# Kernel optimization log

Measured on AMD Instinct MI355X. Metric: run time of the kernel, lower is better.

## Reference

```python
import jax, jax.numpy as jnp
import numpy as np
import itertools

# hyperparameters (match init_kwargs cfg)
V_SIZE = 32000; D = 768; H = 12; NL = 2
K_BITS = 4; L_TAB = 4; M_COPIES = 2; HID = 3072
DK = D // H; R = 1 << K_BITS; EPS = 1e-6; RMS_EPS = 1e-5

def _protos_T():
    # corners of the {-1,+1}^K hypercube, transposed -> [K, R]
    corners = np.array(list(itertools.product([-1.0, 1.0], repeat=K_BITS)), dtype=np.float32)
    return jnp.asarray(corners.T)

def setup_inputs() -> dict:
    key = jax.random.key(0)
    ks = jax.random.split(key, 14)
    s = 0.02
    return {
        "in_idx": jax.random.randint(ks[0], (1, 1024), 0, V_SIZE),
        "tok_emb": jax.random.normal(ks[1], (V_SIZE, D), jnp.float32) * s,
        "norm1_w": jnp.ones((NL, D), jnp.float32),
        "qw": jax.random.normal(ks[2], (NL, D, D), jnp.float32) * s,
        "kw": jax.random.normal(ks[3], (NL, D, D), jnp.float32) * s,
        "vw": jax.random.normal(ks[4], (NL, D, D), jnp.float32) * s,
        "ow": jax.random.normal(ks[5], (NL, D, D), jnp.float32) * s,
        "ob": jnp.zeros((NL, D), jnp.float32),
        "norm2_w": jnp.ones((NL, D), jnp.float32),
        "ff_w1": jax.random.normal(ks[6], (NL, D, HID), jnp.float32) * s,
        "ff_w2": jax.random.normal(ks[7], (NL, D, HID), jnp.float32) * s,
        "ff_w3": jax.random.normal(ks[8], (NL, HID, D), jnp.float32) * s,
        "final_norm_w": jnp.ones((D,), jnp.float32),
        "out_w": jax.random.normal(ks[9], (D, V_SIZE), jnp.float32) * s,
        "planes_T": jax.random.normal(ks[10], (NL, M_COPIES, DK, L_TAB * K_BITS), jnp.float32),
    }

def _rmsnorm(x, w):
    return x * jax.lax.rsqrt(jnp.mean(x * x, axis=-1, keepdims=True) + RMS_EPS) * w

def _race_attention(h, qw, kw, vw, ow, ob, planes, protos_T):
    B, T, _ = h.shape
    Q = (h @ qw).reshape(B, T, H, DK)
    Kt = (h @ kw).reshape(B, T, H, DK)
    Vt = (h @ vw).reshape(B, T, H, DK)
    # RoPE (split-even/odd, concat halves variant, start position 0)
    theta = 10000.0 ** (-jnp.arange(0, DK, 2, dtype=jnp.float32) / DK)
    freq = jnp.arange(T, dtype=jnp.float32)[:, None] * theta[None, :]  # [T, DK/2]
    sin = jnp.sin(freq)[None, :, None, :]
    cos = jnp.cos(freq)[None, :, None, :]
    def rope(z):
        e, o = z[..., ::2], z[..., 1::2]
        return jnp.concatenate([e * cos - o * sin, e * sin + o * cos], axis=-1)
    Q, Kt = rope(Q), rope(Kt)
    to_hb = lambda z: jnp.transpose(z, (0, 2, 1, 3)).reshape(B * H, T, DK)
    Qh, Kh, Vh = to_hb(Q), to_hb(Kt), to_hb(Vt)
    N = M_COPIES * B * H
    scale = jnp.sqrt(jnp.float32(DK))
    # random-plane projections per model copy m: [M, BH, T, L*K]
    projK = jnp.einsum('ntd,mds->mnts', Kh, planes).reshape(N, T, L_TAB, K_BITS)
    projQ = jnp.einsum('ntd,mds->mnts', Qh, planes).reshape(N, T, L_TAB, K_BITS)
    probsK = jax.nn.softmax((jnp.tanh(projK) / scale) @ protos_T, axis=-1)  # [N,T,L,R]
    probsQ = jax.nn.softmax((jnp.tanh(projQ) / scale) @ protos_T, axis=-1)
    Vn = jnp.broadcast_to(Vh[None], (M_COPIES, B * H, T, DK)).reshape(N, T, DK)
    # causal prefix sums over time
    A_pref = jnp.cumsum(probsK, axis=1)                                     # [N,T,L,R]
    B_pref = jnp.cumsum(probsK[..., None] * Vn[:, :, None, None, :], axis=1)  # [N,T,L,R,DK]
    E_pref = B_pref / (A_pref[..., None] + EPS)
    out2 = jnp.einsum('ntlr,ntlrd->ntd', probsQ, E_pref)                    # [N,T,DK]
    out_h = out2.reshape(M_COPIES, B, H, T, DK).transpose(0, 1, 3, 2, 4)    # [M,B,T,H,DK]
    m = out_h.mean(axis=0)                                                  # [B,T,H,DK]
    # faithful to the source: permute to [B,H,T,DK] then row-major reshape to [B,T,H*DK]
    out = jnp.transpose(m, (0, 2, 1, 3)).reshape(B, T, H * DK)
    return out @ ow + ob

def reference(in_idx, tok_emb, norm1_w, qw, kw, vw, ow, ob, norm2_w,
              ff_w1, ff_w2, ff_w3, final_norm_w, out_w, planes_T):
    protos_T = _protos_T()
    x = tok_emb[in_idx]  # [B,T,D]
    for l in range(NL):
        h = _rmsnorm(x, norm1_w[l])
        x = x + _race_attention(h, qw[l], kw[l], vw[l], ow[l], ob[l], planes_T[l], protos_T)
        h = _rmsnorm(x, norm2_w[l])
        x = x + (jax.nn.silu(h @ ff_w1[l]) * (h @ ff_w2[l])) @ ff_w3[l]
    x = _rmsnorm(x, final_norm_w)
    return x @ out_w  # logits [B,T,V]
```

## Files before the change

### kernel.cpp

```cpp
#include <hip/hip_runtime.h>
#include <hip/hip_bf16.h>

#define T_SEQ 1024
#define D_MODEL 768
#define QKVW 2304
#define NHEAD 12
#define NLAYER 2
#define MCOPY 2
#define HID_DIM 3072
#define VSIZE 32000
#define NCH 32
#define TL 32

typedef __attribute__((ext_vector_type(8))) short short8;
typedef __attribute__((ext_vector_type(4))) float f32x4;

__device__ __forceinline__ short f2bf(float f) {
  unsigned u = __builtin_bit_cast(unsigned, f);
  u = (u + 0x7FFFu + ((u >> 16) & 1u)) >> 16;
  return (short)u;
}

__global__ __launch_bounds__(64) void stc_k(float* __restrict__ stc) {
  int t = blockIdx.x;
  int i = threadIdx.x;
  if (i < 32) {
    float theta = powf(10000.0f, -(float)i / 32.0f);
    float s, c;
    sincosf((float)t * theta, &s, &c);
    stc[t * 64 + 2 * i] = c;
    stc[t * 64 + 2 * i + 1] = s;
  }
}

__global__ __launch_bounds__(256) void embed_norm_k(const int* __restrict__ idx,
                                                    const float* __restrict__ emb,
                                                    const float* __restrict__ w,
                                                    float* __restrict__ x,
                                                    short* __restrict__ out) {
  int t = blockIdx.x, tid = threadIdx.x;
  int r = idx[t];
  float v[3];
  float ss = 0.f;
  #pragma unroll
  for (int j = 0; j < 3; ++j) {
    int i = tid + j * 256;
    float val = emb[(size_t)r * D_MODEL + i];
    x[(size_t)t * D_MODEL + i] = val;
    v[j] = val;
    ss += val * val;
  }
  __shared__ float red[256];
  red[tid] = ss; __syncthreads();
  for (int s = 128; s > 0; s >>= 1) {
    if (tid < s) red[tid] += red[tid + s];
    __syncthreads();
  }
  float inv = rsqrtf(red[0] / (float)D_MODEL + 1e-5f);
  #pragma unroll
  for (int j = 0; j < 3; ++j) {
    int i = tid + j * 256;
    out[(size_t)t * D_MODEL + i] = f2bf(v[j] * inv * w[i]);
  }
}

__global__ __launch_bounds__(256) void add_norm_k(float* __restrict__ x,
                                                  const float* __restrict__ parts,
                                                  int nparts,
                                                  const float* __restrict__ bias,
                                                  const float* __restrict__ w,
                                                  short* __restrict__ out) {
  int t = blockIdx.x, tid = threadIdx.x;
  float v[3];
  float ss = 0.f;
  #pragma unroll
  for (int j = 0; j < 3; ++j) {
    int i = tid + j * 256;
    float val = x[(size_t)t * D_MODEL + i];
    if (bias) val += bias[i];
    for (int p = 0; p < nparts; ++p)
      val += parts[(size_t)p * (T_SEQ * D_MODEL) + (size_t)t * D_MODEL + i];
    v[j] = val;
    ss += val * val;
  }
  __shared__ float red[256];
  red[tid] = ss; __syncthreads();
  for (int s = 128; s > 0; s >>= 1) {
    if (tid < s) red[tid] += red[tid + s];
    __syncthreads();
  }
  float inv = rsqrtf(red[0] / (float)D_MODEL + 1e-5f);
  #pragma unroll
  for (int j = 0; j < 3; ++j) {
    int i = tid + j * 256;
    if (nparts || bias) x[(size_t)t * D_MODEL + i] = v[j];
    out[(size_t)t * D_MODEL + i] = f2bf(v[j] * inv * w[i]);
  }
}

__device__ __forceinline__ void tr_tile(const float* __restrict__ W,
                                        short* __restrict__ WT, int K, int N,
                                        int n0, int k0, int tx, int ty) {
  __shared__ float tile[32][33];
  #pragma unroll
  for (int i = 0; i < 4; ++i)
    tile[ty + 8 * i][tx] = W[(size_t)(k0 + ty + 8 * i) * N + n0 + tx];
  __syncthreads();
  #pragma unroll
  for (int i = 0; i < 4; ++i)
    WT[(size_t)(n0 + ty + 8 * i) * K + k0 + tx] = f2bf(tile[tx][ty + 8 * i]);
}

#define SQ_W  ((size_t)D_MODEL * D_MODEL)
#define FF_W  ((size_t)D_MODEL * HID_DIM)
#define LAYER_W (4 * SQ_W + 3 * FF_W)

__global__ __launch_bounds__(256) void transpose_sq8(const float* __restrict__ qw,
                                                     const float* __restrict__ kw,
                                                     const float* __restrict__ vw,
                                                     const float* __restrict__ ow,
                                                     short* __restrict__ WB) {
  int z = blockIdx.z, layer = z >> 2, which = z & 3;
  const float* W = (which == 0) ? qw : (which == 1) ? kw : (which == 2) ? vw : ow;
  W += (size_t)layer * SQ_W;
  short* WT = WB + (size_t)layer * LAYER_W + (size_t)which * SQ_W;
  tr_tile(W, WT, D_MODEL, D_MODEL, blockIdx.x * 32, blockIdx.y * 32,
          threadIdx.x, threadIdx.y);
}

__global__ __launch_bounds__(256) void transpose_ff12(const float* __restrict__ W1g,
                                                      const float* __restrict__ W2g,
                                                      short* __restrict__ WB) {
  __shared__ float tile[32][33];
  int layer = blockIdx.z;
  const float* W1 = W1g + (size_t)layer * FF_W;
  const float* W2 = W2g + (size_t)layer * FF_W;
  short* WT = WB + (size_t)layer * LAYER_W + 4 * SQ_W;
  int tx = threadIdx.x, ty = threadIdx.y;
  int n0 = blockIdx.x * 32, k0 = blockIdx.y * 32;
  int h0 = n0 >> 1;
  const float* src = (tx < 16) ? (W1 + h0 + tx) : (W2 + h0 + (tx - 16));
  #pragma unroll
  for (int i = 0; i < 4; ++i)
    tile[ty + 8 * i][tx] = src[(size_t)(k0 + ty + 8 * i) * HID_DIM];
  __syncthreads();
  #pragma unroll
  for (int i = 0; i < 4; ++i) {
    int n = ty + 8 * i;
    WT[(size_t)(n0 + n) * D_MODEL + k0 + tx] = f2bf(tile[tx][n]);
  }
}

__global__ __launch_bounds__(256) void transpose_f3(const float* __restrict__ W3g,
                                                    short* __restrict__ WB) {
  int layer = blockIdx.z;
  const float* W = W3g + (size_t)layer * FF_W;
  short* WT = WB + (size_t)layer * LAYER_W + 4 * SQ_W + 2 * FF_W;
  tr_tile(W, WT, HID_DIM, D_MODEL, blockIdx.x * 32, blockIdx.y * 32,
          threadIdx.x, threadIdx.y);
}

__global__ __launch_bounds__(256) void transpose_head(const float* __restrict__ W,
                                                      short* __restrict__ WT) {
  tr_tile(W, WT, D_MODEL, VSIZE, blockIdx.x * 32, blockIdx.y * 32,
          threadIdx.x, threadIdx.y);
}

template<int NROW32>
__device__ __forceinline__ void stage_rows(const short* __restrict__ gbase,
                                           int ldK, short* lds, int tid) {
  #pragma unroll
  for (int j = 0; j < NROW32; ++j) {
    int r = j * 32 + (tid >> 3);
    int s = tid & 7;
    const short* gp = gbase + (size_t)r * ldK + (((s ^ (r & 7))) << 3);
    short* lp = lds + j * 2048 + tid * 8;
    __builtin_amdgcn_global_load_lds((const __attribute__((address_space(1))) void*)gp,
                                     (__attribute__((address_space(3))) void*)lp,
                                     16, 0, 0);
  }
}

__device__ __forceinline__ short8 frag_ld(const short* lds, int row, int sl) {
  return *(const short8*)(lds + row * 64 + ((sl ^ (row & 7)) << 3));
}

template<int MODE>
__global__ __launch_bounds__(256) void gemm_t(const short* __restrict__ A,
                                              const short* __restrict__ Bt,
                                              float* __restrict__ Cf,
                                              short* __restrict__ Cs,
                                              int N, int K) {
  __shared__ short As[2][128 * 64];
  __shared__ short Bs[2][128 * 64];
  int tid = threadIdx.x;
  int lane = tid & 63;
  int wave = tid >> 6;
  int wr = wave >> 1, wc = wave & 1;
  int l15 = lane & 15, kg = lane >> 4;

  int cpx = gridDim.x >> 3;
  int wg = (blockIdx.x & 7) * cpx + (blockIdx.x >> 3);
  int row0 = (wg & 7) * 128;
  int col0 = (wg >> 3) * 128;

  int kn = K / gridDim.y;
  int koff = blockIdx.y * kn;
  const short* Ab = A + (size_t)row0 * K + koff;
  const short* Bb = Bt + (size_t)col0 * K + koff;
  int nt = kn >> 6;

  f32x4 acc[4][4] = {};

  stage_rows<4>(Ab, K, As[0], tid);
  stage_rows<4>(Bb, K, Bs[0], tid);
  __syncthreads();

  int cur = 0;
  for (int t = 0; t < nt; ++t) {
    if (t + 1 < nt) {
      stage_rows<4>(Ab + (t + 1) * 64, K, As[cur ^ 1], tid);
      stage_rows<4>(Bb + (t + 1) * 64, K, Bs[cur ^ 1], tid);
    }
    const short* Ac = As[cur];
    const short* Bc = Bs[cur];
    #pragma unroll
    for (int kk = 0; kk < 2; ++kk) {
      short8 af[4], bf4[4];
      #pragma unroll
      for (int m = 0; m < 4; ++m)
        af[m] = frag_ld(Ac, wr * 64 + m * 16 + l15, 4 * kk + kg);
      #pragma unroll
      for (int n = 0; n < 4; ++n)
        bf4[n] = frag_ld(Bc, wc * 64 + n * 16 + l15, 4 * kk + kg);
      #pragma unroll
      for (int m = 0; m < 4; ++m)
        #pragma unroll
        for (int n = 0; n < 4; ++n)
          acc[m][n] = __builtin_amdgcn_mfma_f32_16x16x32_bf16(af[m], bf4[n], acc[m][n], 0, 0, 0);
    }
    __syncthreads();
    cur ^= 1;
  }

  int rbase = (lane >> 4) * 4;
  if constexpr (MODE == 2) {
    int base = col0 + wc * 64;
    #pragma unroll
    for (int p = 0; p < 2; ++p) {
      int h = (base >> 1) + p * 16 + l15;
      #pragma unroll
      for (int m = 0; m < 4; ++m) {
        #pragma unroll
        for (int r = 0; r < 4; ++r) {
          int row = row0 + wr * 64 + m * 16 + rbase + r;
          float g1 = acc[m][2 * p][r];
          float g2 = acc[m][2 * p + 1][r];
          Cs[(size_t)row * HID_DIM + h] = f2bf((g1 / (1.f + expf(-g1))) * g2);
        }
      }
    }
  } else {
    float* Co = Cf;
    if constexpr (MODE == 1) Co += (size_t)blockIdx.y * T_SEQ * N;
    #pragma unroll
    for (int n = 0; n < 4; ++n) {
      int col = col0 + wc * 64 + n * 16 + l15;
      #pragma unroll
      for (int m = 0; m < 4; ++m) {
        #pragma unroll
        for (int r = 0; r < 4; ++r) {
          int row = row0 + wr * 64 + m * 16 + rbase + r;
          Co[(size_t)row * N + col] = acc[m][n][r];
        }
      }
    }
  }
}

__global__ __launch_bounds__(256) void gemm_head(const short* __restrict__ A,
                                                 const short* __restrict__ Bt,
                                                 float* __restrict__ Cf,
                                                 int N, int K) {
  __shared__ short As[128 * 64];
  __shared__ short Bs[256 * 64];
  int tid = threadIdx.x;
  int lane = tid & 63;
  int wave = tid >> 6;
  int wr = wave >> 1, wc = wave & 1;
  int l15 = lane & 15, kg = lane >> 4;

  int cpx = gridDim.x >> 3;
  int wg = (blockIdx.x & 7) * cpx + (blockIdx.x >> 3);
  int row0 = (wg & 7) * 128;
  int col0 = (wg >> 3) * 256;

  const short* Ab = A + (size_t)row0 * K;
  const short* Bb = Bt + (size_t)col0 * K;
  int nt = K >> 6;

  f32x4 acc[4][8] = {};

  for (int t = 0; t < nt; ++t) {
    stage_rows<4>(Ab + t * 64, K, As, tid);
    stage_rows<8>(Bb + t * 64, K, Bs, tid);
    __syncthreads();
    #pragma unroll
    for (int kk = 0; kk < 2; ++kk) {
      short8 af[4], bf8[8];
      #pragma unroll
      for (int m = 0; m < 4; ++m)
        af[m] = frag_ld(As, wr * 64 + m * 16 + l15, 4 * kk + kg);
      #pragma unroll
      for (int n = 0; n < 8; ++n)
        bf8[n] = frag_ld(Bs, wc * 128 + n * 16 + l15, 4 * kk + kg);
      #pragma unroll
      for (int m = 0; m < 4; ++m)
        #pragma unroll
        for (int n = 0; n < 8; ++n)
          acc[m][n] = __builtin_amdgcn_mfma_f32_16x16x32_bf16(af[m], bf8[n], acc[m][n], 0, 0, 0);
    }
    __syncthreads();
  }

  int rbase = (lane >> 4) * 4;
  #pragma unroll
  for (int n = 0; n < 8; ++n) {
    int col = col0 + wc * 128 + n * 16 + l15;
    #pragma unroll
    for (int m = 0; m < 4; ++m) {
      #pragma unroll
      for (int r = 0; r < 4; ++r) {
        int row = row0 + wr * 64 + m * 16 + rbase + r;
        Cf[(size_t)row * N + col] = acc[m][n][r];
      }
    }
  }
}

__global__ __launch_bounds__(256) void race_probs(const float* __restrict__ qkv,
                                                  const float* __restrict__ stc,
                                                  const float* __restrict__ planes,
                                                  float* __restrict__ pq,
                                                  float* __restrict__ pk) {
  int gid = blockIdx.x * 256 + threadIdx.x;
  int w = gid & 1;
  int l = (gid >> 1) & 3;
  int t = (gid >> 3) & 1023;
  int mn = gid >> 13;
  int m = mn / NHEAD, n = mn % NHEAD;
  const float* raw = qkv + (size_t)t * QKVW + (w ? 0 : D_MODEL) + n * 64;
  const float* sc = stc + t * 64;
  const float* pl = planes + m * 64 * 16 + l * 4;
  float p0 = 0.f, p1 = 0.f, p2 = 0.f, p3 = 0.f;
  #pragma unroll 4
  for (int i = 0; i < 32; ++i) {
    float e = raw[2 * i], o = raw[2 * i + 1];
    float c = sc[2 * i], s = sc[2 * i + 1];
    float re = e * c - o * s;
    float ro = e * s + o * c;
    const float* pe = pl + i * 16;
    const float* po = pl + (i + 32) * 16;
    p0 += re * pe[0] + ro * po[0];
    p1 += re * pe[1] + ro * po[1];
    p2 += re * pe[2] + ro * po[2];
    p3 += re * pe[3] + ro * po[3];
  }
  float t0 = tanhf(p0) * 0.125f;
  float t1 = tanhf(p1) * 0.125f;
  float t2 = tanhf(p2) * 0.125f;
  float t3 = tanhf(p3) * 0.125f;
  float lg[16];
  float mx = -1e30f;
  #pragma unroll
  for (int r = 0; r < 16; ++r) {
    float s = ((r & 8) ? t0 : -t0) + ((r & 4) ? t1 : -t1) +
              ((r & 2) ? t2 : -t2) + ((r & 1) ? t3 : -t3);
    lg[r] = s;
    mx = fmaxf(mx, s);
  }
  float sum = 0.f;
  #pragma unroll
  for (int r = 0; r < 16; ++r) {
    float e = expf(lg[r] - mx);
    lg[r] = e;
    sum += e;
  }
  float inv = 1.f / sum;
  float* dst = (w ? pq : pk) + ((size_t)mn * T_SEQ + t) * 64 + l * 16;
  #pragma unroll
  for (int r = 0; r < 16; ++r) dst[r] = lg[r] * inv;
}

__global__ __launch_bounds__(256) void race_chunksum(const float* __restrict__ pk_g,
                                                     const float* __restrict__ v_g,
                                                     float* __restrict__ csA,
                                                     float* __restrict__ csB) {
  int mn = blockIdx.x, ch = blockIdx.y;
  int n = mn % NHEAD;
  int tid = threadIdx.x;
  int d = tid & 63, g = tid >> 6;
  __shared__ float pk[64], vv[64];
  float a[16], bp[16];
  #pragma unroll
  for (int i = 0; i < 16; ++i) { a[i] = 0.f; bp[i] = 0.f; }
  const float* pkrow = pk_g + ((size_t)mn * T_SEQ + (size_t)ch * TL) * 64;
  const float* vrow = v_g + (size_t)(ch * TL) * QKVW + n * 64;
  for (int t = 0; t < TL; ++t) {
    if (tid < 64) pk[tid] = pkrow[t * 64 + tid];
    else if (tid < 128) vv[tid - 64] = vrow[(size_t)t * QKVW + tid - 64];
    __syncthreads();
    float vd = vv[d];
    #pragma unroll
    for (int i = 0; i < 16; ++i) {
      float p = pk[g * 16 + i];
      a[i] += p;
      bp[i] = fmaf(p, vd, bp[i]);
    }
    __syncthreads();
  }
  size_t base = ((size_t)mn * NCH + ch) * 64;
  if (d == 0) {
    #pragma unroll
    for (int i = 0; i < 16; ++i) csA[base + g * 16 + i] = a[i];
  }
  #pragma unroll
  for (int i = 0; i < 16; ++i) csB[(base + g * 16 + i) * 64 + d] = bp[i];
}

__global__ __launch_bounds__(64) void race_chunkscan(float* __restrict__ csA,
                                                     float* __restrict__ csB) {
  int mn = blockIdx.x, lr = blockIdx.y;
  int d = threadIdx.x;
  float runB = 0.f, runA = 0.f;
  for (int c = 0; c < NCH; ++c) {
    size_t ib = (((size_t)mn * NCH + c) * 64 + lr) * 64 + d;
    float b = csB[ib];
    csB[ib] = runB;
    runB += b;
    if (d == 0) {
      size_t ia = ((size_t)mn * NCH + c) * 64 + lr;
      float av = csA[ia];
      csA[ia] = runA;
      runA += av;
    }
  }
}

__global__ __launch_bounds__(256) void race_scan_emit(const float* __restrict__ pk_g,
                                                      const float* __restrict__ pq_g,
                                                      const float* __restrict__ v_g,
                                                      const float* __restrict__ csA,
                                                      const float* __restrict__ csB,
                                                      short* __restrict__ ro) {
  int n = blockIdx.x, ch = blockIdx.y;
  int tid = threadIdx.x;
  int d = tid & 63, g = tid >> 6;
  int mn0 = n, mn1 = NHEAD + n;
  __shared__ float pk0[64], pk1[64], pq0[64], pq1[64], vv[64];
  __shared__ float part[4][64];
  float a0[16], b0[16], a1[16], b1[16];
  size_t base0 = ((size_t)mn0 * NCH + ch) * 64;
  size_t base1 = ((size_t)mn1 * NCH + ch) * 64;
  #pragma unroll
  for (int i = 0; i < 16; ++i) {
    a0[i] = csA[base0 + g * 16 + i];
    b0[i] = csB[(base0 + g * 16 + i) * 64 + d];
    a1[i] = csA[base1 + g * 16 + i];
    b1[i] = csB[(base1 + g * 16 + i) * 64 + d];
  }
  const float* pk0r = pk_g + ((size_t)mn0 * T_SEQ + (size_t)ch * TL) * 64;
  const float* pk1r = pk_g + ((size_t)mn1 * T_SEQ + (size_t)ch * TL) * 64;
  const float* pq0r = pq_g + ((size_t)mn0 * T_SEQ + (size_t)ch * TL) * 64;
  const float* pq1r = pq_g + ((size_t)mn1 * T_SEQ + (size_t)ch * TL) * 64;
  const float* vrow = v_g + (size_t)(ch * TL) * QKVW + n * 64;
  for (int t = 0; t < TL; ++t) {
    if (g == 0) { pk0[d] = pk0r[t * 64 + d]; vv[d] = vrow[(size_t)t * QKVW + d]; }
    else if (g == 1) pk1[d] = pk1r[t * 64 + d];
    else if (g == 2) pq0[d] = pq0r[t * 64 + d];
    else pq1[d] = pq1r[t * 64 + d];
    __syncthreads();
    float vd = vv[d];
    float c = 0.f;
    #pragma unroll
    for (int i = 0; i < 16; ++i) {
      int lr = g * 16 + i;
      float p = pk0[lr];
      a0[i] += p;
      b0[i] = fmaf(p, vd, b0[i]);
      c = fmaf(pq0[lr] * b0[i], __builtin_amdgcn_rcpf(a0[i] + 1e-6f), c);
      p = pk1[lr];
      a1[i] += p;
      b1[i] = fmaf(p, vd, b1[i]);
      c = fmaf(pq1[lr] * b1[i], __builtin_amdgcn_rcpf(a1[i] + 1e-6f), c);
    }
    part[g][d] = c;
    __syncthreads();
    if (tid < 64) {
      float s = part[0][tid] + part[1][tid] + part[2][tid] + part[3][tid];
      ro[n * (T_SEQ * 64) + (ch * TL + t) * 64 + tid] = f2bf(0.5f * s);
    }
  }
}

extern "C" void kernel_launch(void* const* d_in, const int* in_sizes, int n_in,
                              void* d_out, int out_size, void* d_ws, size_t ws_size,
                              hipStream_t stream) {
  const int*   in_idx       = (const int*)d_in[0];
  const float* tok_emb      = (const float*)d_in[1];
  const float* norm1_w      = (const float*)d_in[2];
  const float* qw           = (const float*)d_in[3];
  const float* kw           = (const float*)d_in[4];
  const float* vw           = (const float*)d_in[5];
  const float* ow           = (const float*)d_in[6];
  const float* ob           = (const float*)d_in[7];
  const float* norm2_w      = (const float*)d_in[8];
  const float* ff_w1        = (const float*)d_in[9];
  const float* ff_w2        = (const float*)d_in[10];
  const float* ff_w3        = (const float*)d_in[11];
  const float* final_norm_w = (const float*)d_in[12];
  const float* out_w        = (const float*)d_in[13];
  const float* planes       = (const float*)d_in[14];

  float* ws = (float*)d_ws;
  const size_t SZ_TD = (size_t)T_SEQ * D_MODEL;
  float* X   = ws;
  float* STC = X + SZ_TD;
  float* S   = STC + 65536;
  short* HbB = (short*)S;
  float* QKV = S + 393216;
  float* PK  = QKV + (size_t)T_SEQ * QKVW;
  float* PQ  = PK + (size_t)MCOPY * NHEAD * T_SEQ * 64;
  float* CSA = PQ + (size_t)MCOPY * NHEAD * T_SEQ * 64;
  float* CSB = CSA + (size_t)MCOPY * NHEAD * NCH * 64;
  short* ROb = (short*)(CSB + (size_t)MCOPY * NHEAD * NCH * 64 * 64);
  short* G1B = (short*)QKV;
  float* PP  = PK;
  short* WB = (short*)(S + 9486336);
  short* outT = WB + NLAYER * LAYER_W;

  stc_k<<<T_SEQ, 64, 0, stream>>>(STC);
  dim3 tb(32, 8);
  transpose_sq8<<<dim3(24, 24, 8), tb, 0, stream>>>(qw, kw, vw, ow, WB);
  transpose_ff12<<<dim3(192, 24, 2), tb, 0, stream>>>(ff_w1, ff_w2, WB);
  transpose_f3<<<dim3(24, 96, 2), tb, 0, stream>>>(ff_w3, WB);
  transpose_head<<<dim3(1000, 24), tb, 0, stream>>>(out_w, outT);

  embed_norm_k<<<T_SEQ, 256, 0, stream>>>(in_idx, tok_emb, norm1_w, X, HbB);

  for (int l = 0; l < NLAYER; ++l) {
    short* base = WB + (size_t)l * LAYER_W;
    short* qkvT = base;
    short* owT  = base + 3 * SQ_W;
    short* f12T = base + 4 * SQ_W;
    short* f3T  = base + 4 * SQ_W + 2 * FF_W;

    gemm_t<0><<<dim3(8 * (QKVW / 128), 1), 256, 0, stream>>>(HbB, qkvT, QKV, nullptr, QKVW, D_MODEL);
    race_probs<<<(MCOPY * NHEAD * T_SEQ * 4 * 2) / 256, 256, 0, stream>>>(
        QKV, STC, planes + (size_t)l * MCOPY * 64 * 16, PQ, PK);
    dim3 gps(MCOPY * NHEAD, NCH);
    race_chunksum<<<gps, 256, 0, stream>>>(PK, QKV + 2 * D_MODEL, CSA, CSB);
    dim3 gcs(MCOPY * NHEAD, 64);
    race_chunkscan<<<gcs, 64, 0, stream>>>(CSA, CSB);
    dim3 gemit(NHEAD, NCH);
    race_scan_emit<<<gemit, 256, 0, stream>>>(PK, PQ, QKV + 2 * D_MODEL, CSA, CSB, ROb);
    gemm_t<1><<<dim3(8 * (D_MODEL / 128), 2), 256, 0, stream>>>(ROb, owT, PP, nullptr, D_MODEL, D_MODEL);
    add_norm_k<<<T_SEQ, 256, 0, stream>>>(X, PP, 2, ob + l * D_MODEL, norm2_w + l * D_MODEL, HbB);
    gemm_t<2><<<dim3(8 * (2 * HID_DIM / 128), 1), 256, 0, stream>>>(HbB, f12T, nullptr, G1B, 2 * HID_DIM, D_MODEL);
    gemm_t<1><<<dim3(8 * (D_MODEL / 128), 4), 256, 0, stream>>>(G1B, f3T, PP, nullptr, D_MODEL, HID_DIM);
    const float* nw = (l == NLAYER - 1) ? final_norm_w : norm1_w + (l + 1) * D_MODEL;
    add_norm_k<<<T_SEQ, 256, 0, stream>>>(X, PP, 4, nullptr, nw, HbB);
  }
  gemm_head<<<8 * (VSIZE / 256), 256, 0, stream>>>(HbB, outT, (float*)d_out, VSIZE, D_MODEL);
}
```

Before: 528.0 us.

## Add 64x128 GEMM tile, single-buffer head GEMM, restructure RACE scan kernels

Adds a gemm64 kernel with 64x128 tiles and double buffering, used for the QKV, output-projection and FF3 GEMMs so more workgroups fill the GPU. The LM head now uses the 128x128 gemm_t in a new single-buffered mode in place of the 128x256 gemm_head. The chunksum and scan_emit kernels prefetch the next row into registers with double-buffered LDS, dropping one barrier per step, and scan_emit reduces partial sums with wave shuffles instead of an LDS pass. Smaller tiles cut data reuse per tile, and the smaller head tile re-reads A more often.

```diff
diff --git a/kernel.cpp b/kernel.cpp
--- a/kernel.cpp
+++ b/kernel.cpp
@@ -185,14 +185,14 @@
   return *(const short8*)(lds + row * 64 + ((sl ^ (row & 7)) << 3));
 }
 
-template<int MODE>
+template<int MODE, int DBUF>
 __global__ __launch_bounds__(256) void gemm_t(const short* __restrict__ A,
                                               const short* __restrict__ Bt,
                                               float* __restrict__ Cf,
                                               short* __restrict__ Cs,
                                               int N, int K) {
-  __shared__ short As[2][128 * 64];
-  __shared__ short Bs[2][128 * 64];
+  __shared__ short As[DBUF + 1][128 * 64];
+  __shared__ short Bs[DBUF + 1][128 * 64];
   int tid = threadIdx.x;
   int lane = tid & 63;
   int wave = tid >> 6;
@@ -212,15 +212,23 @@
 
   f32x4 acc[4][4] = {};
 
-  stage_rows<4>(Ab, K, As[0], tid);
-  stage_rows<4>(Bb, K, Bs[0], tid);
-  __syncthreads();
+  if constexpr (DBUF) {
+    stage_rows<4>(Ab, K, As[0], tid);
+    stage_rows<4>(Bb, K, Bs[0], tid);
+    __syncthreads();
+  }
 
   int cur = 0;
   for (int t = 0; t < nt; ++t) {
-    if (t + 1 < nt) {
-      stage_rows<4>(Ab + (t + 1) * 64, K, As[cur ^ 1], tid);
-      stage_rows<4>(Bb + (t + 1) * 64, K, Bs[cur ^ 1], tid);
+    if constexpr (DBUF) {
+      if (t + 1 < nt) {
+        stage_rows<4>(Ab + (t + 1) * 64, K, As[cur ^ 1], tid);
+        stage_rows<4>(Bb + (t + 1) * 64, K, Bs[cur ^ 1], tid);
+      }
+    } else {
+      stage_rows<4>(Ab + t * 64, K, As[0], tid);
+      stage_rows<4>(Bb + t * 64, K, Bs[0], tid);
+      __syncthreads();
     }
     const short* Ac = As[cur];
     const short* Bc = Bs[cur];
@@ -240,7 +248,7 @@
           acc[m][n] = __builtin_amdgcn_mfma_f32_16x16x32_bf16(af[m], bf4[n], acc[m][n], 0, 0, 0);
     }
     __syncthreads();
-    cur ^= 1;
+    if constexpr (DBUF) cur ^= 1;
   }
 
   int rbase = (lane >> 4) * 4;
@@ -278,61 +286,74 @@
   }
 }
 
-__global__ __launch_bounds__(256) void gemm_head(const short* __restrict__ A,
-                                                 const short* __restrict__ Bt,
-                                                 float* __restrict__ Cf,
-                                                 int N, int K) {
-  __shared__ short As[128 * 64];
-  __shared__ short Bs[256 * 64];
+template<int MODE>
+__global__ __launch_bounds__(256) void gemm64(const short* __restrict__ A,
+                                              const short* __restrict__ Bt,
+                                              float* __restrict__ Cf,
+                                              int N, int K) {
+  __shared__ short As[2][64 * 64];
+  __shared__ short Bs[2][128 * 64];
   int tid = threadIdx.x;
   int lane = tid & 63;
   int wave = tid >> 6;
-  int wr = wave >> 1, wc = wave & 1;
   int l15 = lane & 15, kg = lane >> 4;
 
   int cpx = gridDim.x >> 3;
   int wg = (blockIdx.x & 7) * cpx + (blockIdx.x >> 3);
-  int row0 = (wg & 7) * 128;
-  int col0 = (wg >> 3) * 256;
-
-  const short* Ab = A + (size_t)row0 * K;
-  const short* Bb = Bt + (size_t)col0 * K;
-  int nt = K >> 6;
-
-  f32x4 acc[4][8] = {};
-
+  int row0 = (wg & 15) * 64;
+  int col0 = (wg >> 4) * 128;
+
+  int kn = K / gridDim.y;
+  int koff = blockIdx.y * kn;
+  const short* Ab = A + (size_t)row0 * K + koff;
+  const short* Bb = Bt + (size_t)col0 * K + koff;
+  int nt = kn >> 6;
+
+  f32x4 acc[4][2] = {};
+
+  stage_rows<2>(Ab, K, As[0], tid);
+  stage_rows<4>(Bb, K, Bs[0], tid);
+  __syncthreads();
+
+  int cur = 0;
   for (int t = 0; t < nt; ++t) {
-    stage_rows<4>(Ab + t * 64, K, As, tid);
-    stage_rows<8>(Bb + t * 64, K, Bs, tid);
-    __syncthreads();
+    if (t + 1 < nt) {
+      stage_rows<2>(Ab + (t + 1) * 64, K, As[cur ^ 1], tid);
+      stage_rows<4>(Bb + (t + 1) * 64, K, Bs[cur ^ 1], tid);
+    }
+    const short* Ac = As[cur];
+    const short* Bc = Bs[cur];
     #pragma unroll
     for (int kk = 0; kk < 2; ++kk) {
-      short8 af[4], bf8[8];
+      short8 af[4], bf2[2];
       #pragma unroll
       for (int m = 0; m < 4; ++m)
-        af[m] = frag_ld(As, wr * 64 + m * 16 + l15, 4 * kk + kg);
-      #pragma unroll
-      for (int n = 0; n < 8; ++n)
-        bf8[n] = frag_ld(Bs, wc * 128 + n * 16 + l15, 4 * kk + kg);
+        af[m] = frag_ld(Ac, m * 16 + l15, 4 * kk + kg);
+      #pragma unroll
+      for (int n = 0; n < 2; ++n)
+        bf2[n] = frag_ld(Bc, wave * 32 + n * 16 + l15, 4 * kk + kg);
       #pragma unroll
       for (int m = 0; m < 4; ++m)
         #pragma unroll
-        for (int n = 0; n < 8; ++n)
-          acc[m][n] = __builtin_amdgcn_mfma_f32_16x16x32_bf16(af[m], bf8[n], acc[m][n], 0, 0, 0);
+        for (int n = 0; n < 2; ++n)
+          acc[m][n] = __builtin_amdgcn_mfma_f32_16x16x32_bf16(af[m], bf2[n], acc[m][n], 0, 0, 0);
     }
     __syncthreads();
+    cur ^= 1;
   }
 
   int rbase = (lane >> 4) * 4;
-  #pragma unroll
-  for (int n = 0; n < 8; ++n) {
-    int col = col0 + wc * 128 + n * 16 + l15;
+  float* Co = Cf;
+  if constexpr (MODE == 1) Co += (size_t)blockIdx.y * T_SEQ * N;
+  #pragma unroll
+  for (int n = 0; n < 2; ++n) {
+    int col = col0 + wave * 32 + n * 16 + l15;
     #pragma unroll
     for (int m = 0; m < 4; ++m) {
       #pragma unroll
       for (int r = 0; r < 4; ++r) {
-        int row = row0 + wr * 64 + m * 16 + rbase + r;
-        Cf[(size_t)row * N + col] = acc[m][n][r];
+        int row = row0 + m * 16 + rbase + r;
+        Co[(size_t)row * N + col] = acc[m][n][r];
       }
     }
   }
@@ -399,28 +420,41 @@
   int mn = blockIdx.x, ch = blockIdx.y;
   int n = mn % NHEAD;
   int tid = threadIdx.x;
-  int d = tid & 63, g = tid >> 6;
-  __shared__ float pk[64], vv[64];
-  float a[16], bp[16];
-  #pragma unroll
-  for (int i = 0; i < 16; ++i) { a[i] = 0.f; bp[i] = 0.f; }
+  int wave = tid >> 6, lane = tid & 63;
+  int l15 = lane & 15, g = lane >> 4;
+  int d = wave * 16 + l15;
+  __shared__ float L[2][2][64];
   const float* pkrow = pk_g + ((size_t)mn * T_SEQ + (size_t)ch * TL) * 64;
   const float* vrow = v_g + (size_t)(ch * TL) * QKVW + n * 64;
+
+  float a[16], bp[16];
+  #pragma unroll
+  for (int i = 0; i < 16; ++i) { a[i] = 0.f; bp[i] = 0.f; }
+
+  float r0 = 0.f;
+  if (wave == 0) r0 = pkrow[lane];
+  else if (wave == 1) r0 = vrow[lane];
+
+  int cur = 0;
+  #pragma unroll 1
   for (int t = 0; t < TL; ++t) {
-    if (tid < 64) pk[tid] = pkrow[t * 64 + tid];
-    else if (tid < 128) vv[tid - 64] = vrow[(size_t)t * QKVW + tid - 64];
+    if (wave < 2) L[cur][wave][lane] = r0;
     __syncthreads();
-    float vd = vv[d];
+    if (t + 1 < TL) {
+      if (wave == 0) r0 = pkrow[(t + 1) * 64 + lane];
+      else if (wave == 1) r0 = vrow[(size_t)(t + 1) * QKVW + lane];
+    }
+    float vd = L[cur][1][d];
     #pragma unroll
     for (int i = 0; i < 16; ++i) {
-      float p = pk[g * 16 + i];
+      float p = L[cur][0][g * 16 + i];
       a[i] += p;
       bp[i] = fmaf(p, vd, bp[i]);
     }
-    __syncthreads();
+    cur ^= 1;
   }
   size_t base = ((size_t)mn * NCH + ch) * 64;
-  if (d == 0) {
+  if (wave == 0 && l15 == 0) {
     #pragma unroll
     for (int i = 0; i < 16; ++i) csA[base + g * 16 + i] = a[i];
   }
@@ -455,10 +489,20 @@
                                                       short* __restrict__ ro) {
   int n = blockIdx.x, ch = blockIdx.y;
   int tid = threadIdx.x;
-  int d = tid & 63, g = tid >> 6;
+  int wave = tid >> 6, lane = tid & 63;
+  int l15 = lane & 15, g = lane >> 4;
+  int d = wave * 16 + l15;
   int mn0 = n, mn1 = NHEAD + n;
-  __shared__ float pk0[64], pk1[64], pq0[64], pq1[64], vv[64];
-  __shared__ float part[4][64];
+  __shared__ float L[2][5][64];
+
+  const float* pk0r = pk_g + ((size_t)mn0 * T_SEQ + (size_t)ch * TL) * 64;
+  const float* pk1r = pk_g + ((size_t)mn1 * T_SEQ + (size_t)ch * TL) * 64;
+  const float* pq0r = pq_g + ((size_t)mn0 * T_SEQ + (size_t)ch * TL) * 64;
+  const float* pq1r = pq_g + ((size_t)mn1 * T_SEQ + (size_t)ch * TL) * 64;
+  const float* vrow = v_g + (size_t)(ch * TL) * QKVW + n * 64;
+  const float* src0 = (wave == 0) ? pk0r : (wave == 1) ? pk1r
+                    : (wave == 2) ? pq0r : pq1r;
+
   float a0[16], b0[16], a1[16], b1[16];
   size_t base0 = ((size_t)mn0 * NCH + ch) * 64;
   size_t base1 = ((size_t)mn1 * NCH + ch) * 64;
@@ -469,37 +513,39 @@
     a1[i] = csA[base1 + g * 16 + i];
     b1[i] = csB[(base1 + g * 16 + i) * 64 + d];
   }
-  const float* pk0r = pk_g + ((size_t)mn0 * T_SEQ + (size_t)ch * TL) * 64;
-  const float* pk1r = pk_g + ((size_t)mn1 * T_SEQ + (size_t)ch * TL) * 64;
-  const float* pq0r = pq_g + ((size_t)mn0 * T_SEQ + (size_t)ch * TL) * 64;
-  const float* pq1r = pq_g + ((size_t)mn1 * T_SEQ + (size_t)ch * TL) * 64;
-  const float* vrow = v_g + (size_t)(ch * TL) * QKVW + n * 64;
+
+  float r0 = src0[lane];
+  float r1 = (wave == 0) ? vrow[lane] : 0.f;
+
+  int cur = 0;
+  #pragma unroll 1
   for (int t = 0; t < TL; ++t) {
-    if (g == 0) { pk0[d] = pk0r[t * 64 + d]; vv[d] = vrow[(size_t)t * QKVW + d]; }
-    else if (g == 1) pk1[d] = pk1r[t * 64 + d];
-    else if (g == 2) pq0[d] = pq0r[t * 64 + d];
-    else pq1[d] = pq1r[t * 64 + d];
+    L[cur][wave][lane] = r0;
+    if (wave == 0) L[cur][4][lane] = r1;
     __syncthreads();
-    float vd = vv[d];
+    if (t + 1 < TL) {
+      r0 = src0[(t + 1) * 64 + lane];
+      if (wave == 0) r1 = vrow[(size_t)(t + 1) * QKVW + lane];
+    }
+    float vd = L[cur][4][d];
     float c = 0.f;
     #pragma unroll
     for (int i = 0; i < 16; ++i) {
       int lr = g * 16 + i;
-      float p = pk0[lr];
+      float p = L[cur][0][lr];
       a0[i] += p;
       b0[i] = fmaf(p, vd, b0[i]);
-      c = fmaf(pq0[lr] * b0[i], __builtin_amdgcn_rcpf(a0[i] + 1e-6f), c);
-      p = pk1[lr];
+      c = fmaf(L[cur][2][lr] * b0[i], __builtin_amdgcn_rcpf(a0[i] + 1e-6f), c);
+      p = L[cur][1][lr];
       a1[i] += p;
       b1[i] = fmaf(p, vd, b1[i]);
-      c = fmaf(pq1[lr] * b1[i], __builtin_amdgcn_rcpf(a1[i] + 1e-6f), c);
-    }
-    part[g][d] = c;
-    __syncthreads();
-    if (tid < 64) {
-      float s = part[0][tid] + part[1][tid] + part[2][tid] + part[3][tid];
-      ro[n * (T_SEQ * 64) + (ch * TL + t) * 64 + tid] = f2bf(0.5f * s);
-    }
+      c = fmaf(L[cur][3][lr] * b1[i], __builtin_amdgcn_rcpf(a1[i] + 1e-6f), c);
+    }
+    c += __shfl_xor(c, 16);
+    c += __shfl_xor(c, 32);
+    if (g == 0)
+      ro[n * (T_SEQ * 64) + (ch * TL + t) * 64 + d] = f2bf(0.5f * c);
+    cur ^= 1;
   }
 }
 
@@ -555,7 +601,7 @@
     short* f12T = base + 4 * SQ_W;
     short* f3T  = base + 4 * SQ_W + 2 * FF_W;
 
-    gemm_t<0><<<dim3(8 * (QKVW / 128), 1), 256, 0, stream>>>(HbB, qkvT, QKV, nullptr, QKVW, D_MODEL);
+    gemm64<0><<<dim3(16 * (QKVW / 128), 1), 256, 0, stream>>>(HbB, qkvT, QKV, QKVW, D_MODEL);
     race_probs<<<(MCOPY * NHEAD * T_SEQ * 4 * 2) / 256, 256, 0, stream>>>(
         QKV, STC, planes + (size_t)l * MCOPY * 64 * 16, PQ, PK);
     dim3 gps(MCOPY * NHEAD, NCH);
@@ -564,12 +610,12 @@
     race_chunkscan<<<gcs, 64, 0, stream>>>(CSA, CSB);
     dim3 gemit(NHEAD, NCH);
     race_scan_emit<<<gemit, 256, 0, stream>>>(PK, PQ, QKV + 2 * D_MODEL, CSA, CSB, ROb);
-    gemm_t<1><<<dim3(8 * (D_MODEL / 128), 2), 256, 0, stream>>>(ROb, owT, PP, nullptr, D_MODEL, D_MODEL);
+    gemm64<1><<<dim3(16 * (D_MODEL / 128), 2), 256, 0, stream>>>(ROb, owT, PP, D_MODEL, D_MODEL);
     add_norm_k<<<T_SEQ, 256, 0, stream>>>(X, PP, 2, ob + l * D_MODEL, norm2_w + l * D_MODEL, HbB);
-    gemm_t<2><<<dim3(8 * (2 * HID_DIM / 128), 1), 256, 0, stream>>>(HbB, f12T, nullptr, G1B, 2 * HID_DIM, D_MODEL);
-    gemm_t<1><<<dim3(8 * (D_MODEL / 128), 4), 256, 0, stream>>>(G1B, f3T, PP, nullptr, D_MODEL, HID_DIM);
+    gemm_t<2, 1><<<dim3(8 * (2 * HID_DIM / 128), 1), 256, 0, stream>>>(HbB, f12T, nullptr, G1B, 2 * HID_DIM, D_MODEL);
+    gemm64<1><<<dim3(16 * (D_MODEL / 128), 4), 256, 0, stream>>>(G1B, f3T, PP, D_MODEL, HID_DIM);
     const float* nw = (l == NLAYER - 1) ? final_norm_w : norm1_w + (l + 1) * D_MODEL;
     add_norm_k<<<T_SEQ, 256, 0, stream>>>(X, PP, 4, nullptr, nw, HbB);
   }
-  gemm_head<<<8 * (VSIZE / 256), 256, 0, stream>>>(HbB, outT, (float*)d_out, VSIZE, D_MODEL);
-}
+  gemm_t<0, 0><<<dim3(8 * (VSIZE / 128), 1), 256, 0, stream>>>(HbB, outT, (float*)d_out, nullptr, VSIZE, D_MODEL);
+}
```

After: 466.3 us. 1.13x faster.
